# Performance work log

Measured on AMD Instinct MI355X. Metric: run time of the kernel, lower is better.

Reference implementation:

```python
import jax, jax.numpy as jnp
import numpy as np

B, T = 4096, 1024
IN, H, N, OUT = 1, 40, 40, 1  # input_size, hidden_size, nr_nodes, output_size
SLOPE = 0.01  # LeakyReLU negative slope (torch default)


def setup_inputs() -> dict:
    key = jax.random.key(0)
    ks = jax.random.split(key, 9)
    s = lambda fan_in: 1.0 / np.sqrt(fan_in)
    u = lambda k, shape, fan_in: jax.random.uniform(k, shape, jnp.float32, -s(fan_in), s(fan_in))
    return {
        "inputs": jax.random.normal(ks[0], (B, T), dtype=jnp.float32),
        # H2H: Linear(41->40), LeakyReLU, Linear(40->40)
        "h2h_w1": u(ks[1], (N, IN + H), IN + H),
        "h2h_b1": u(ks[2], (N,), IN + H),
        "h2h_w2": u(ks[3], (H, N), N),
        "h2h_b2": u(ks[4], (H,), N),
        # H2O: Linear(41->40), LeakyReLU, Linear(40->1)
        "h2o_w1": u(ks[5], (N, IN + H), IN + H),
        "h2o_b1": u(ks[6], (N,), IN + H),
        "h2o_w2": u(ks[7], (OUT, N), N),
        "h2o_b2": u(ks[8], (OUT,), N),
    }


def reference(inputs, h2h_w1, h2h_b1, h2h_w2, h2h_b2, h2o_w1, h2o_b1, h2o_w2, h2o_b2):
    def step(hidden, u_t):
        # combined: [B, 1+H]
        combined = jnp.concatenate([u_t[:, None], hidden], axis=1)
        a = jax.nn.leaky_relu(combined @ h2h_w1.T + h2h_b1, SLOPE)
        hidden_new = a @ h2h_w2.T + h2h_b2                      # [B, H]
        o = jax.nn.leaky_relu(combined @ h2o_w1.T + h2o_b1, SLOPE)
        out_t = (o @ h2o_w2.T + h2o_b2)[:, 0]                   # [B]
        return hidden_new, out_t

    hidden0 = jnp.zeros((inputs.shape[0], H), dtype=inputs.dtype)
    _, ys = jax.lax.scan(step, hidden0, inputs.T)  # ys: [T, B]
    return ys.T  # [B, T]
```

## Files before the change

### kernel.cpp

```cpp
#include <hip/hip_runtime.h>
#include <hip/hip_bf16.h>


#define B_SZ 4096
#define T_SZ 1024
#define HID  40
#define WSTRIDE 88

typedef unsigned short u16;
typedef unsigned int   u32;
typedef float f2 __attribute__((ext_vector_type(2)));
typedef float f4 __attribute__((ext_vector_type(4)));

#define WFENCE() do {                      \
    asm volatile("" ::: "memory");         \
    __builtin_amdgcn_wave_barrier();       \
    asm volatile("" ::: "memory");         \
  } while (0)

__device__ __forceinline__ float bf2f(u16 v) {
  union { u32 u; float f; } c; c.u = ((u32)v) << 16; return c.f;
}

__device__ __forceinline__ bool detect_bf16(const void* w) {
  const u16* p = (const u16*)w;
  bool bf = true;
  for (int i = 0; i < 64; ++i) {
    float f = bf2f(p[i]);
    if (!(fabsf(f) <= 0.2f)) bf = false;
  }
  return bf;
}

__device__ __forceinline__ float ldgr(bool bf, const void* p, long i) {
  return bf ? bf2f(((const u16*)p)[i]) : ((const float*)p)[i];
}

__device__ __forceinline__ float pair_other(float x) {
  return __int_as_float(__builtin_amdgcn_update_dpp(
      0, __float_as_int(x), 0xB1, 0xF, 0xF, true));
}

__global__ __launch_bounds__(64)
void pack_weights(const void* __restrict__ h2h_w1, const void* __restrict__ h2h_b1,
                  const void* __restrict__ h2h_w2, const void* __restrict__ h2h_b2,
                  const void* __restrict__ h2o_w1, const void* __restrict__ h2o_b1,
                  const void* __restrict__ h2o_w2, const void* __restrict__ h2o_b2,
                  float* __restrict__ ws) {
  const bool bf  = detect_bf16(h2h_w1);
  const int lane = threadIdx.x;
  const int kh   = lane & 1;
  const int w    = lane >> 1;
  const int koff = kh * 20;

  const bool hh01 = (2 * w < HID);
  const void* p01 = hh01 ? h2h_w1 : h2o_w1;
  const long  jr0 = hh01 ? 2 * w : 2 * w - HID;
  const bool  s2A = (w >= 16);
  const void* p2  = s2A ? h2o_w1 : h2h_w2;
  const long  o2  = s2A ? ((long)(8 + w) * 41 + 1 + koff) : ((long)w * HID + koff);
  const bool  isOut = (w == 24);
  const void* p3  = isOut ? h2o_w2 : h2h_w2;
  const long  o3  = isOut ? (long)koff : ((long)(16 + (w < 24 ? w : 0)) * HID + koff);

  float* dst = ws + (long)lane * WSTRIDE;
  for (int i = 0; i < 20; ++i) {
    dst[i]      = ldgr(bf, p01, jr0 * 41 + 1 + koff + i);
    dst[20 + i] = ldgr(bf, p01, (jr0 + 1) * 41 + 1 + koff + i);
    dst[40 + i] = ldgr(bf, p2, o2 + i);
    dst[60 + i] = ldgr(bf, p3, o3 + i);
  }
  float wu0 = 0, wu1 = 0, wu2 = 0, ba0 = 0, ba1 = 0, ba2 = 0, bb2 = 0, bb3 = 0;
  if (kh == 0) {
    const void* b1p = hh01 ? h2h_b1 : h2o_b1;
    wu0 = ldgr(bf, p01, jr0 * 41);
    wu1 = ldgr(bf, p01, (jr0 + 1) * 41);
    ba0 = ldgr(bf, b1p, jr0);
    ba1 = ldgr(bf, b1p, jr0 + 1);
    if (s2A) { wu2 = ldgr(bf, h2o_w1, (long)(8 + w) * 41); ba2 = ldgr(bf, h2o_b1, 8 + w); }
    else     { bb2 = ldgr(bf, h2h_b2, w); }
    if (isOut)       bb3 = ldgr(bf, h2o_b2, 0);
    else if (w < 24) bb3 = ldgr(bf, h2h_b2, 16 + w);
  }
  dst[80] = wu0; dst[81] = wu1; dst[82] = wu2; dst[83] = ba0;
  dst[84] = ba1; dst[85] = ba2; dst[86] = bb2; dst[87] = bb3;
}

template <bool BF>
__global__ __launch_bounds__(64)
__attribute__((amdgpu_waves_per_eu(4, 4)))
void rnn_kernel(const void* __restrict__ inp, const void* __restrict__ h2h_w1,
                const float* __restrict__ ws, void* __restrict__ out) {
  __shared__ __align__(16) float sH[44];
  __shared__ __align__(16) float sA[84];

  if (detect_bf16(h2h_w1) != BF) return;

  const int lane = threadIdx.x & 63;
  const int kh   = lane & 1;
  const int w    = lane >> 1;
  const int koff = kh * 20;
  const bool s2A   = (w >= 16);
  const bool isOut = (w == 24);

  f4 wq[20];
  {
    const f4* src = (const f4*)(ws + (long)lane * WSTRIDE);
#pragma unroll
    for (int i = 0; i < 20; ++i) wq[i] = src[i];
  }
  asm volatile("" :
      "+v"(wq[0]),  "+v"(wq[1]),  "+v"(wq[2]),  "+v"(wq[3]),  "+v"(wq[4]),
      "+v"(wq[5]),  "+v"(wq[6]),  "+v"(wq[7]),  "+v"(wq[8]),  "+v"(wq[9]),
      "+v"(wq[10]), "+v"(wq[11]), "+v"(wq[12]), "+v"(wq[13]), "+v"(wq[14]),
      "+v"(wq[15]), "+v"(wq[16]), "+v"(wq[17]), "+v"(wq[18]), "+v"(wq[19]));
  const f2* wp = (const f2*)wq;

  const float* wsc = ws + (long)lane * WSTRIDE + 80;
  const float wu0 = wsc[0], wu1 = wsc[1], wu2 = wsc[2], ba0 = wsc[3];
  const float ba1 = wsc[4], ba2 = wsc[5], bb2 = wsc[6], bb3 = wsc[7];

  for (int i = lane; i < 44; i += 64) sH[i] = 0.f;
  WFENCE();

  const long base = (long)blockIdx.x * T_SZ;
  float u_cur = BF ? bf2f(((const u16*)inp)[base]) : ((const float*)inp)[base];

  const f4* hp = (const f4*)(&sH[koff]);
  const f4* ap = (const f4*)(&sA[isOut ? 40 + koff : koff]);
  const bool wrA2 = s2A && (kh == 0);
  const bool wr2  = (!s2A) && (kh == 0);
  const bool wr3  = (w < 24) && (kh == 0);
  const bool wrY  = isOut && (kh == 0);

  for (int t = 0; t < T_SZ; ++t) {
    const float u_nxt = (t + 1 < T_SZ)
        ? (BF ? bf2f(((const u16*)inp)[base + t + 1]) : ((const float*)inp)[base + t + 1])
        : 0.f;

    {
      f2 a0 = {0.f, 0.f}, a1 = {0.f, 0.f}, a2 = {0.f, 0.f};
#pragma unroll
      for (int m = 0; m < 5; ++m) {
        const f4 h4 = hp[m];
        const f2 hA = {h4.x, h4.y}, hB = {h4.z, h4.w};
        a0 = hA * wp[2 * m]      + a0;
        a0 = hB * wp[2 * m + 1]  + a0;
        a1 = hA * wp[10 + 2 * m] + a1;
        a1 = hB * wp[11 + 2 * m] + a1;
        a2 = hA * wp[20 + 2 * m] + a2;
        a2 = hB * wp[21 + 2 * m] + a2;
      }
      const float v0 = fmaf(u_cur, wu0, ba0) + a0.x + a0.y;
      const float v1 = fmaf(u_cur, wu1, ba1) + a1.x + a1.y;
      const float v2 = fmaf(u_cur, wu2, ba2) + a2.x + a2.y;
      const float t0 = v0 + pair_other(v0);
      const float t1 = v1 + pair_other(v1);
      const float t2 = v2 + pair_other(v2);
      if (kh == 0) {
        f2 act01;
        act01.x = fmaxf(t0, 0.01f * t0);
        act01.y = fmaxf(t1, 0.01f * t1);
        *(f2*)(&sA[2 * w]) = act01;
      }
      if (wrA2) sA[48 + w] = fmaxf(t2, 0.01f * t2);
    }
    WFENCE();

    {
      f2 b2 = {0.f, 0.f}, b3 = {0.f, 0.f};
#pragma unroll
      for (int m = 0; m < 5; ++m) {
        const f4 a4 = ap[m];
        const f2 aA = {a4.x, a4.y}, aB = {a4.z, a4.w};
        b2 = aA * wp[20 + 2 * m] + b2;
        b2 = aB * wp[21 + 2 * m] + b2;
        b3 = aA * wp[30 + 2 * m] + b3;
        b3 = aB * wp[31 + 2 * m] + b3;
      }
      const float v2 = bb2 + b2.x + b2.y;
      const float v3 = bb3 + b3.x + b3.y;
      const float t2 = v2 + pair_other(v2);
      const float t3 = v3 + pair_other(v3);
      if (wr2) sH[w] = t2;
      if (wr3) sH[16 + w] = t3;
      if (wrY) {
        if (BF) ((__hip_bfloat16*)out)[base + t] = __float2bfloat16(t3);
        else    ((float*)out)[base + t] = t3;
      }
    }
    WFENCE();

    u_cur = u_nxt;
  }
}

extern "C" void kernel_launch(void* const* d_in, const int* in_sizes, int n_in,
                              void* d_out, int out_size, void* d_ws, size_t ws_size,
                              hipStream_t stream) {
  (void)in_sizes; (void)n_in; (void)out_size;
  if (ws_size < (size_t)(64 * WSTRIDE * sizeof(float))) return;
  float* ws = (float*)d_ws;
  pack_weights<<<dim3(1), dim3(64), 0, stream>>>(
      d_in[1], d_in[2], d_in[3], d_in[4],
      d_in[5], d_in[6], d_in[7], d_in[8], ws);
  rnn_kernel<false><<<dim3(B_SZ), dim3(64), 0, stream>>>(
      d_in[0], d_in[1], ws, d_out);
  rnn_kernel<true><<<dim3(B_SZ), dim3(64), 0, stream>>>(
      d_in[0], d_in[1], ws, d_out);
}
```

Before: 864.5 us.

## Process two batch rows per wavefront to raise ILP in recurrent loop

Each 64-lane block now advances two independent sequences at once, with double shared-memory buffers for hidden state and activations, and launches half as many blocks. Interleaving two independent dot-product chains is meant to hide the latency of the serial per-step dependency and the wave barriers. Weights are no longer pinned in registers: they are reread through a pointer each step, relying on the compiler or cache to keep them close. The waves-per-EU hint is removed, which trades occupancy for register headroom.

```diff
diff --git a/kernel.cpp b/kernel.cpp
--- a/kernel.cpp
+++ b/kernel.cpp
@@ -88,11 +88,10 @@
 
 template <bool BF>
 __global__ __launch_bounds__(64)
-__attribute__((amdgpu_waves_per_eu(4, 4)))
 void rnn_kernel(const void* __restrict__ inp, const void* __restrict__ h2h_w1,
                 const float* __restrict__ ws, void* __restrict__ out) {
-  __shared__ __align__(16) float sH[44];
-  __shared__ __align__(16) float sA[84];
+  __shared__ __align__(16) float sH[2][44];
+  __shared__ __align__(16) float sA[2][84];
 
   if (detect_bf16(h2h_w1) != BF) return;
 
@@ -103,95 +102,126 @@
   const bool s2A   = (w >= 16);
   const bool isOut = (w == 24);
 
-  f4 wq[20];
-  {
-    const f4* src = (const f4*)(ws + (long)lane * WSTRIDE);
-#pragma unroll
-    for (int i = 0; i < 20; ++i) wq[i] = src[i];
-  }
-  asm volatile("" :
-      "+v"(wq[0]),  "+v"(wq[1]),  "+v"(wq[2]),  "+v"(wq[3]),  "+v"(wq[4]),
-      "+v"(wq[5]),  "+v"(wq[6]),  "+v"(wq[7]),  "+v"(wq[8]),  "+v"(wq[9]),
-      "+v"(wq[10]), "+v"(wq[11]), "+v"(wq[12]), "+v"(wq[13]), "+v"(wq[14]),
-      "+v"(wq[15]), "+v"(wq[16]), "+v"(wq[17]), "+v"(wq[18]), "+v"(wq[19]));
-  const f2* wp = (const f2*)wq;
-
+  const f4* wq = (const f4*)(ws + (long)lane * WSTRIDE);
   const float* wsc = ws + (long)lane * WSTRIDE + 80;
   const float wu0 = wsc[0], wu1 = wsc[1], wu2 = wsc[2], ba0 = wsc[3];
   const float ba1 = wsc[4], ba2 = wsc[5], bb2 = wsc[6], bb3 = wsc[7];
 
-  for (int i = lane; i < 44; i += 64) sH[i] = 0.f;
+  for (int i = lane; i < 2 * 44; i += 64) ((float*)sH)[i] = 0.f;
   WFENCE();
 
-  const long base = (long)blockIdx.x * T_SZ;
-  float u_cur = BF ? bf2f(((const u16*)inp)[base]) : ((const float*)inp)[base];
-
-  const f4* hp = (const f4*)(&sH[koff]);
-  const f4* ap = (const f4*)(&sA[isOut ? 40 + koff : koff]);
+  const long base0 = (long)(blockIdx.x * 2) * T_SZ;
+  const long base1 = base0 + T_SZ;
+  float u0 = BF ? bf2f(((const u16*)inp)[base0]) : ((const float*)inp)[base0];
+  float u1 = BF ? bf2f(((const u16*)inp)[base1]) : ((const float*)inp)[base1];
+
+  const f4* hp0 = (const f4*)(&sH[0][koff]);
+  const f4* hp1 = (const f4*)(&sH[1][koff]);
+  const f4* ap0 = (const f4*)(&sA[0][isOut ? 40 + koff : koff]);
+  const f4* ap1 = (const f4*)(&sA[1][isOut ? 40 + koff : koff]);
   const bool wrA2 = s2A && (kh == 0);
   const bool wr2  = (!s2A) && (kh == 0);
   const bool wr3  = (w < 24) && (kh == 0);
   const bool wrY  = isOut && (kh == 0);
 
   for (int t = 0; t < T_SZ; ++t) {
-    const float u_nxt = (t + 1 < T_SZ)
-        ? (BF ? bf2f(((const u16*)inp)[base + t + 1]) : ((const float*)inp)[base + t + 1])
-        : 0.f;
+    const float u0n = (t + 1 < T_SZ)
+        ? (BF ? bf2f(((const u16*)inp)[base0 + t + 1]) : ((const float*)inp)[base0 + t + 1]) : 0.f;
+    const float u1n = (t + 1 < T_SZ)
+        ? (BF ? bf2f(((const u16*)inp)[base1 + t + 1]) : ((const float*)inp)[base1 + t + 1]) : 0.f;
 
     {
-      f2 a0 = {0.f, 0.f}, a1 = {0.f, 0.f}, a2 = {0.f, 0.f};
+      f2 a00 = {0,0}, a10 = {0,0}, a20 = {0,0};
+      f2 a01 = {0,0}, a11 = {0,0}, a21 = {0,0};
 #pragma unroll
       for (int m = 0; m < 5; ++m) {
-        const f4 h4 = hp[m];
-        const f2 hA = {h4.x, h4.y}, hB = {h4.z, h4.w};
-        a0 = hA * wp[2 * m]      + a0;
-        a0 = hB * wp[2 * m + 1]  + a0;
-        a1 = hA * wp[10 + 2 * m] + a1;
-        a1 = hB * wp[11 + 2 * m] + a1;
-        a2 = hA * wp[20 + 2 * m] + a2;
-        a2 = hB * wp[21 + 2 * m] + a2;
-      }
-      const float v0 = fmaf(u_cur, wu0, ba0) + a0.x + a0.y;
-      const float v1 = fmaf(u_cur, wu1, ba1) + a1.x + a1.y;
-      const float v2 = fmaf(u_cur, wu2, ba2) + a2.x + a2.y;
-      const float t0 = v0 + pair_other(v0);
-      const float t1 = v1 + pair_other(v1);
-      const float t2 = v2 + pair_other(v2);
-      if (kh == 0) {
-        f2 act01;
-        act01.x = fmaxf(t0, 0.01f * t0);
-        act01.y = fmaxf(t1, 0.01f * t1);
-        *(f2*)(&sA[2 * w]) = act01;
-      }
-      if (wrA2) sA[48 + w] = fmaxf(t2, 0.01f * t2);
+        const f4 w0 = wq[m], w1 = wq[5 + m], w2 = wq[10 + m];
+        const f4 h0 = hp0[m], h1 = hp1[m];
+        const f2 h0A = {h0.x, h0.y}, h0B = {h0.z, h0.w};
+        const f2 h1A = {h1.x, h1.y}, h1B = {h1.z, h1.w};
+        const f2 w0A = {w0.x, w0.y}, w0B = {w0.z, w0.w};
+        const f2 w1A = {w1.x, w1.y}, w1B = {w1.z, w1.w};
+        const f2 w2A = {w2.x, w2.y}, w2B = {w2.z, w2.w};
+        a00 = h0A * w0A + a00;  a01 = h1A * w0A + a01;
+        a00 = h0B * w0B + a00;  a01 = h1B * w0B + a01;
+        a10 = h0A * w1A + a10;  a11 = h1A * w1A + a11;
+        a10 = h0B * w1B + a10;  a11 = h1B * w1B + a11;
+        a20 = h0A * w2A + a20;  a21 = h1A * w2A + a21;
+        a20 = h0B * w2B + a20;  a21 = h1B * w2B + a21;
+      }
+      {
+        const float v0 = fmaf(u0, wu0, ba0) + a00.x + a00.y;
+        const float v1 = fmaf(u0, wu1, ba1) + a10.x + a10.y;
+        const float v2 = fmaf(u0, wu2, ba2) + a20.x + a20.y;
+        const float t0 = v0 + pair_other(v0);
+        const float t1 = v1 + pair_other(v1);
+        const float t2 = v2 + pair_other(v2);
+        if (kh == 0) {
+          f2 act; act.x = fmaxf(t0, 0.01f * t0); act.y = fmaxf(t1, 0.01f * t1);
+          *(f2*)(&sA[0][2 * w]) = act;
+        }
+        if (wrA2) sA[0][48 + w] = fmaxf(t2, 0.01f * t2);
+      }
+      {
+        const float v0 = fmaf(u1, wu0, ba0) + a01.x + a01.y;
+        const float v1 = fmaf(u1, wu1, ba1) + a11.x + a11.y;
+        const float v2 = fmaf(u1, wu2, ba2) + a21.x + a21.y;
+        const float t0 = v0 + pair_other(v0);
+        const float t1 = v1 + pair_other(v1);
+        const float t2 = v2 + pair_other(v2);
+        if (kh == 0) {
+          f2 act; act.x = fmaxf(t0, 0.01f * t0); act.y = fmaxf(t1, 0.01f * t1);
+          *(f2*)(&sA[1][2 * w]) = act;
+        }
+        if (wrA2) sA[1][48 + w] = fmaxf(t2, 0.01f * t2);
+      }
     }
     WFENCE();
 
     {
-      f2 b2 = {0.f, 0.f}, b3 = {0.f, 0.f};
+      f2 b20 = {0,0}, b30 = {0,0};
+      f2 b21 = {0,0}, b31 = {0,0};
 #pragma unroll
       for (int m = 0; m < 5; ++m) {
-        const f4 a4 = ap[m];
-        const f2 aA = {a4.x, a4.y}, aB = {a4.z, a4.w};
-        b2 = aA * wp[20 + 2 * m] + b2;
-        b2 = aB * wp[21 + 2 * m] + b2;
-        b3 = aA * wp[30 + 2 * m] + b3;
-        b3 = aB * wp[31 + 2 * m] + b3;
-      }
-      const float v2 = bb2 + b2.x + b2.y;
-      const float v3 = bb3 + b3.x + b3.y;
-      const float t2 = v2 + pair_other(v2);
-      const float t3 = v3 + pair_other(v3);
-      if (wr2) sH[w] = t2;
-      if (wr3) sH[16 + w] = t3;
-      if (wrY) {
-        if (BF) ((__hip_bfloat16*)out)[base + t] = __float2bfloat16(t3);
-        else    ((float*)out)[base + t] = t3;
+        const f4 w2 = wq[10 + m], w3 = wq[15 + m];
+        const f4 a0 = ap0[m], a1 = ap1[m];
+        const f2 a0A = {a0.x, a0.y}, a0B = {a0.z, a0.w};
+        const f2 a1A = {a1.x, a1.y}, a1B = {a1.z, a1.w};
+        const f2 w2A = {w2.x, w2.y}, w2B = {w2.z, w2.w};
+        const f2 w3A = {w3.x, w3.y}, w3B = {w3.z, w3.w};
+        b20 = a0A * w2A + b20;  b21 = a1A * w2A + b21;
+        b20 = a0B * w2B + b20;  b21 = a1B * w2B + b21;
+        b30 = a0A * w3A + b30;  b31 = a1A * w3A + b31;
+        b30 = a0B * w3B + b30;  b31 = a1B * w3B + b31;
+      }
+      {
+        const float v2 = bb2 + b20.x + b20.y;
+        const float v3 = bb3 + b30.x + b30.y;
+        const float t2 = v2 + pair_other(v2);
+        const float t3 = v3 + pair_other(v3);
+        if (wr2) sH[0][w] = t2;
+        if (wr3) sH[0][16 + w] = t3;
+        if (wrY) {
+          if (BF) ((__hip_bfloat16*)out)[base0 + t] = __float2bfloat16(t3);
+          else    ((float*)out)[base0 + t] = t3;
+        }
+      }
+      {
+        const float v2 = bb2 + b21.x + b21.y;
+        const float v3 = bb3 + b31.x + b31.y;
+        const float t2 = v2 + pair_other(v2);
+        const float t3 = v3 + pair_other(v3);
+        if (wr2) sH[1][w] = t2;
+        if (wr3) sH[1][16 + w] = t3;
+        if (wrY) {
+          if (BF) ((__hip_bfloat16*)out)[base1 + t] = __float2bfloat16(t3);
+          else    ((float*)out)[base1 + t] = t3;
+        }
       }
     }
     WFENCE();
 
-    u_cur = u_nxt;
+    u0 = u0n; u1 = u1n;
   }
 }
 
@@ -204,8 +234,8 @@
   pack_weights<<<dim3(1), dim3(64), 0, stream>>>(
       d_in[1], d_in[2], d_in[3], d_in[4],
       d_in[5], d_in[6], d_in[7], d_in[8], ws);
-  rnn_kernel<false><<<dim3(B_SZ), dim3(64), 0, stream>>>(
+  rnn_kernel<false><<<dim3(B_SZ / 2), dim3(64), 0, stream>>>(
       d_in[0], d_in[1], ws, d_out);
-  rnn_kernel<true><<<dim3(B_SZ), dim3(64), 0, stream>>>(
+  rnn_kernel<true><<<dim3(B_SZ / 2), dim3(64), 0, stream>>>(
       d_in[0], d_in[1], ws, d_out);
 }
```

New measurement: 1.590 ms. +84.0%, slower.
